# Performance work log

Measured on AMD Instinct MI355X. Metric: run time of the kernel, lower is better.

The kernel has to match this reference:

```python
import jax, jax.numpy as jnp
import numpy as np

B, T, M, VM = 64, 512, 8, 50  # batch, time, num_modules, rois per module
EPS = 1e-5  # BatchNorm eps


def setup_inputs() -> dict:
    key = jax.random.key(0)
    ks = jax.random.split(key, 12)
    x = jax.random.normal(ks[0], (B, M * VM, T, 1), jnp.float32)
    # learned adjacency, torch init = ones/V; perturb slightly
    PA = jnp.full((M, VM, VM), 1.0 / VM, jnp.float32) + 0.01 * jax.random.normal(ks[1], (M, VM, VM), jnp.float32)
    conv_w = jax.random.normal(ks[2], (M,), jnp.float32)          # 1x1 conv weight (1->1 chan) per module
    conv_b = 0.1 * jax.random.normal(ks[3], (M,), jnp.float32)
    bn_gamma = 1.0 + 0.1 * jax.random.normal(ks[4], (M,), jnp.float32)
    bn_beta = 0.1 * jax.random.normal(ks[5], (M,), jnp.float32)
    bn_mean = 0.1 * jax.random.normal(ks[6], (M,), jnp.float32)
    bn_var = jax.random.uniform(ks[7], (M,), jnp.float32) + 0.5   # positive
    w1 = jax.random.normal(ks[8], (M, 8), jnp.float32) * 0.5      # Linear(1,8) weight per module
    b1 = 0.1 * jax.random.normal(ks[9], (M, 8), jnp.float32)
    w2 = jax.random.normal(ks[10], (M, 8), jnp.float32) * 0.5     # Linear(8,1) weight per module
    b2 = 0.1 * jax.random.normal(ks[11], (M,), jnp.float32)
    return dict(x=x, PA=PA, conv_w=conv_w, conv_b=conv_b, bn_gamma=bn_gamma, bn_beta=bn_beta,
                bn_mean=bn_mean, bn_var=bn_var, w1=w1, b1=b1, w2=w2, b2=b2)


def reference(x, PA, conv_w, conv_b, bn_gamma, bn_beta, bn_mean, bn_var, w1, b1, w2, b2):
    # x: [B, V_total, T, 1]; torch permute(0,3,2,1) -> [B, C=1, T, V_total]
    xp = x[..., 0].transpose(0, 2, 1)                 # [B, T, V_total]
    xm = xp.reshape(B, T, M, VM)                      # contiguous module blocks == index_select
    # UnitGCN: x_agg = x @ A per module
    agg = jnp.einsum('btmv,mvw->btmw', xm, PA)        # [B, T, M, VM]
    # 1x1 conv (scalar per module) + BatchNorm2d(1) in eval mode + ReLU
    y = agg * conv_w[:, None] + conv_b[:, None]
    scale = bn_gamma / jnp.sqrt(bn_var + EPS)
    h = jax.nn.relu((y - bn_mean[:, None]) * scale[:, None] + bn_beta[:, None])
    # AttentionPooling: MLP(1->8->1) on channel dim, softmax over nodes, weighted sum
    hid = jnp.tanh(h[..., None] * w1[:, None, :] + b1[:, None, :])   # [B, T, M, VM, 8]
    score = jnp.einsum('btmvh,mh->btmv', hid, w2) + b2[:, None]      # [B, T, M, VM]
    attn = jax.nn.softmax(score, axis=3)
    pooled = jnp.sum(h * attn, axis=3)                # [B, T, M]
    # concat over modules on dim 1 -> [B, M, T, 1]
    return pooled.transpose(0, 2, 1)[..., None]
```

## Files before the change

### kernel.cpp

```cpp
#include <hip/hip_runtime.h>

#define BB 64
#define TT 512
#define MM 8
#define VMM 50
#define TBLK 128
#define RSTRIDE 36
#define EPSV 1e-5f

#define TN   1024
#define HMAX 16.0f
#define HSTEP (HMAX / TN)
#define INVH  (TN / HMAX)

using short8  = __attribute__((ext_vector_type(8))) short;
using float4v = __attribute__((ext_vector_type(4))) float;

__device__ __forceinline__ float fast_rcp(float x) {
    return __builtin_amdgcn_rcpf(x);
}
__device__ __forceinline__ float fast_tanh(float x) {
    float e2 = __expf(2.0f * x);
    return fmaf(-2.0f, fast_rcp(e2 + 1.0f), 1.0f);
}
__device__ __forceinline__ unsigned f2bf(float f) {
    unsigned u = __float_as_uint(f);
    return (u + 0x7FFFu + ((u >> 16) & 1u)) >> 16;
}
__device__ __forceinline__ unsigned pack2(float lo, float hi) {
    return f2bf(lo) | (f2bf(hi) << 16);
}
__device__ __forceinline__ unsigned packh2(float lo, float hi) {
    unsigned short a = __builtin_bit_cast(unsigned short, (_Float16)lo);
    unsigned short b = __builtin_bit_cast(unsigned short, (_Float16)hi);
    return (unsigned)a | ((unsigned)b << 16);
}
__device__ __forceinline__ float h2f_lo(unsigned p) {
    return (float)__builtin_bit_cast(_Float16, (unsigned short)(p & 0xFFFFu));
}
__device__ __forceinline__ float h2f_hi(unsigned p) {
    return (float)__builtin_bit_cast(_Float16, (unsigned short)(p >> 16));
}

__global__ __launch_bounds__(256)
__attribute__((amdgpu_waves_per_eu(4, 4)))
void intra_module_agg_kernel(const float* __restrict__ x,
                             const float* __restrict__ PA,
                             const float* __restrict__ conv_w,
                             const float* __restrict__ conv_b,
                             const float* __restrict__ bn_gamma,
                             const float* __restrict__ bn_beta,
                             const float* __restrict__ bn_mean,
                             const float* __restrict__ bn_var,
                             const float* __restrict__ w1,
                             const float* __restrict__ b1,
                             const float* __restrict__ w2,
                             const float* __restrict__ b2,
                             float* __restrict__ out)
{
    const int blk = blockIdx.x;
    const int tq  = blk & 3;
    const int m   = (blk >> 2) & 7;
    const int b   = blk >> 5;
    const int j   = threadIdx.x;

    const int lane = j & 63, wv = j >> 6;
    const int q = lane >> 4, nl = lane & 15;

    __shared__ __align__(16) unsigned psu[64 * RSTRIDE];
    __shared__ __align__(16) unsigned gt[TN];

    const float scale = bn_gamma[m] * __frsqrt_rn(bn_var[m] + EPSV);
    const float Amul  = conv_w[m] * scale;
    const float Cadd  = (conv_b[m] - bn_mean[m]) * scale + bn_beta[m];

    const int t0 = tq * TBLK;
    float xr[2][16];
#pragma unroll
    for (int t2 = 0; t2 < 2; ++t2) {
        const int t = t0 + (wv * 2 + t2) * 16 + nl;
        const float* xg = x + ((b * (MM * VMM) + m * VMM) * TT + t);
#pragma unroll
        for (int jj = 0; jj < 8; ++jj) {
            xr[t2][jj] = xg[(q * 8 + jj) * TT];
        }
#pragma unroll
        for (int jj = 0; jj < 8; ++jj) {
            int v  = 32 + q * 8 + jj;
            int vc = (v < VMM) ? v : 0;
            float tv = xg[vc * TT];
            xr[t2][8 + jj] = (v < VMM) ? tv : 0.0f;
        }
    }

    {
        const float* pa = PA + m * (VMM * VMM);
        const int w  = j & 63;
        const int vb = (j >> 6) * 8;
#pragma unroll
        for (int i = 0; i < 8; ++i) {
            int vp = vb + i, v0 = 2 * vp, v1 = v0 + 1;
            float a = (w < VMM && v0 < VMM) ? pa[v0 * VMM + w] : 0.0f;
            float c = (w < VMM && v1 < VMM) ? pa[v1 * VMM + w] : 0.0f;
            psu[w * RSTRIDE + vp] = pack2(a, c);
        }
    }

    {
        float W1[8], B1[8], W2[8];
        float B2 = b2[m], sabs = 0.0f;
#pragma unroll
        for (int k = 0; k < 8; ++k) {
            W1[k] = w1[m * 8 + k];
            B1[k] = b1[m * 8 + k];
            W2[k] = w2[m * 8 + k];
            sabs += fabsf(W2[k]);
        }
        const float s0 = (B2 + sabs) - 8.0f;
        float gv[5];
#pragma unroll
        for (int k = 0; k < 5; ++k) {
            float h = (4 * j + k) * HSTEP;
            float s = B2 - s0;
#pragma unroll
            for (int i = 0; i < 8; ++i)
                s = fmaf(W2[i], fast_tanh(fmaf(h, W1[i], B1[i])), s);
            gv[k] = __expf(s);
        }
#pragma unroll
        for (int k = 0; k < 4; ++k)
            gt[4 * j + k] = packh2(gv[k], gv[k + 1] - gv[k]);
    }

    short8 Bf[2][2];
#pragma unroll
    for (int t2 = 0; t2 < 2; ++t2) {
#pragma unroll
        for (int ks = 0; ks < 2; ++ks) {
            uint4 u;
            u.x = pack2(xr[t2][8 * ks + 0], xr[t2][8 * ks + 1]);
            u.y = pack2(xr[t2][8 * ks + 2], xr[t2][8 * ks + 3]);
            u.z = pack2(xr[t2][8 * ks + 4], xr[t2][8 * ks + 5]);
            u.w = pack2(xr[t2][8 * ks + 6], xr[t2][8 * ks + 7]);
            Bf[t2][ks] = __builtin_bit_cast(short8, u);
        }
    }

    __syncthreads();

    short8 A[4][2];
#pragma unroll
    for (int wt = 0; wt < 4; ++wt)
#pragma unroll
        for (int ks = 0; ks < 2; ++ks)
            A[wt][ks] = *(const short8*)&psu[(wt * 16 + nl) * RSTRIDE + ks * 16 + q * 4];

    float4v C[2][4];
#pragma unroll
    for (int t2 = 0; t2 < 2; ++t2)
#pragma unroll
        for (int wt = 0; wt < 4; ++wt)
            C[t2][wt] = (float4v){0.f, 0.f, 0.f, 0.f};

#pragma unroll
    for (int t2 = 0; t2 < 2; ++t2) {
#pragma unroll
        for (int wt = 0; wt < 4; ++wt) {
            C[t2][wt] = __builtin_amdgcn_mfma_f32_16x16x32_bf16(A[wt][0], Bf[t2][0], C[t2][wt], 0, 0, 0);
            C[t2][wt] = __builtin_amdgcn_mfma_f32_16x16x32_bf16(A[wt][1], Bf[t2][1], C[t2][wt], 0, 0, 0);
        }
    }

    const int obase = (b * MM + m) * TT + t0;
#pragma unroll
    for (int t2 = 0; t2 < 2; ++t2) {
        float se = 0.0f, sh = 0.0f;
#pragma unroll
        for (int wt = 0; wt < 4; ++wt) {
#pragma unroll
            for (int r = 0; r < 4; ++r) {
                const int w = wt * 16 + q * 4 + r;
                float h = fmaxf(fmaf(C[t2][wt][r], Amul, Cadd), 0.0f);
                float u = fminf(h, HMAX - 0.0005f) * INVH;
                int   i = (int)u;
                float fr = u - (float)i;
                unsigned p = gt[i];
                float e = (w < VMM) ? fmaf(fr, h2f_hi(p), h2f_lo(p)) : 0.0f;
                se += e;
                sh = fmaf(h, e, sh);
            }
        }
        se += __shfl_xor(se, 16, 64);
        se += __shfl_xor(se, 32, 64);
        sh += __shfl_xor(sh, 16, 64);
        sh += __shfl_xor(sh, 32, 64);
        if (q == 0)
            out[obase + (wv * 2 + t2) * 16 + nl] = sh * fast_rcp(se);
    }
}

extern "C" void kernel_launch(void* const* d_in, const int* in_sizes, int n_in,
                              void* d_out, int out_size, void* d_ws, size_t ws_size,
                              hipStream_t stream) {
    const float* x        = (const float*)d_in[0];
    const float* PA       = (const float*)d_in[1];
    const float* conv_w   = (const float*)d_in[2];
    const float* conv_b   = (const float*)d_in[3];
    const float* bn_gamma = (const float*)d_in[4];
    const float* bn_beta  = (const float*)d_in[5];
    const float* bn_mean  = (const float*)d_in[6];
    const float* bn_var   = (const float*)d_in[7];
    const float* w1       = (const float*)d_in[8];
    const float* b1       = (const float*)d_in[9];
    const float* w2       = (const float*)d_in[10];
    const float* b2       = (const float*)d_in[11];
    float* out = (float*)d_out;

    intra_module_agg_kernel<<<dim3(BB * MM * (TT / TBLK)), dim3(256), 0, stream>>>(
        x, PA, conv_w, conv_b, bn_gamma, bn_beta, bn_mean, bn_var,
        w1, b1, w2, b2, out);
}
```

Measured before the change: 115.2 us.

## Process full time axis per block with double-buffered register prefetch

Each block now handles all 512 timesteps of one (batch, module) pair instead of a 128-step quarter. The PA staging and exp lookup-table setup are done once per four tiles instead of once per tile. The next tile's loads are issued into a second register bank while the current tile runs its MFMA and softmax work. The grid shrinks from 2048 to 512 blocks and the waves-per-EU hint is relaxed to allow more registers, which may reduce occupancy and latency hiding.

```diff
diff --git a/kernel.cpp b/kernel.cpp
--- a/kernel.cpp
+++ b/kernel.cpp
@@ -4,7 +4,6 @@
 #define TT 512
 #define MM 8
 #define VMM 50
-#define TBLK 128
 #define RSTRIDE 36
 #define EPSV 1e-5f
 
@@ -42,8 +41,43 @@
     return (float)__builtin_bit_cast(_Float16, (unsigned short)(p >> 16));
 }
 
+__device__ __forceinline__ void load_tile(const float* __restrict__ xgb,
+                                          int t0, int wv, int nl, int q,
+                                          float xr[2][16])
+{
+#pragma unroll
+    for (int t2 = 0; t2 < 2; ++t2) {
+        const float* xg = xgb + t0 + (wv * 2 + t2) * 16 + nl;
+#pragma unroll
+        for (int jj = 0; jj < 8; ++jj)
+            xr[t2][jj] = xg[(q * 8 + jj) * TT];
+#pragma unroll
+        for (int jj = 0; jj < 8; ++jj) {
+            int v  = 32 + q * 8 + jj;
+            int vc = (v < VMM) ? v : 0;
+            float tv = xg[vc * TT];
+            xr[t2][8 + jj] = (v < VMM) ? tv : 0.0f;
+        }
+    }
+}
+
+__device__ __forceinline__ void pack_tile(const float xr[2][16], short8 Bf[2][2])
+{
+#pragma unroll
+    for (int t2 = 0; t2 < 2; ++t2)
+#pragma unroll
+        for (int ks = 0; ks < 2; ++ks) {
+            uint4 u;
+            u.x = pack2(xr[t2][8 * ks + 0], xr[t2][8 * ks + 1]);
+            u.y = pack2(xr[t2][8 * ks + 2], xr[t2][8 * ks + 3]);
+            u.z = pack2(xr[t2][8 * ks + 4], xr[t2][8 * ks + 5]);
+            u.w = pack2(xr[t2][8 * ks + 6], xr[t2][8 * ks + 7]);
+            Bf[t2][ks] = __builtin_bit_cast(short8, u);
+        }
+}
+
 __global__ __launch_bounds__(256)
-__attribute__((amdgpu_waves_per_eu(4, 4)))
+__attribute__((amdgpu_waves_per_eu(2)))
 void intra_module_agg_kernel(const float* __restrict__ x,
                              const float* __restrict__ PA,
                              const float* __restrict__ conv_w,
@@ -59,9 +93,8 @@
                              float* __restrict__ out)
 {
     const int blk = blockIdx.x;
-    const int tq  = blk & 3;
-    const int m   = (blk >> 2) & 7;
-    const int b   = blk >> 5;
+    const int m   = blk & 7;
+    const int b   = blk >> 3;
     const int j   = threadIdx.x;
 
     const int lane = j & 63, wv = j >> 6;
@@ -74,24 +107,11 @@
     const float Amul  = conv_w[m] * scale;
     const float Cadd  = (conv_b[m] - bn_mean[m]) * scale + bn_beta[m];
 
-    const int t0 = tq * TBLK;
-    float xr[2][16];
-#pragma unroll
-    for (int t2 = 0; t2 < 2; ++t2) {
-        const int t = t0 + (wv * 2 + t2) * 16 + nl;
-        const float* xg = x + ((b * (MM * VMM) + m * VMM) * TT + t);
-#pragma unroll
-        for (int jj = 0; jj < 8; ++jj) {
-            xr[t2][jj] = xg[(q * 8 + jj) * TT];
-        }
-#pragma unroll
-        for (int jj = 0; jj < 8; ++jj) {
-            int v  = 32 + q * 8 + jj;
-            int vc = (v < VMM) ? v : 0;
-            float tv = xg[vc * TT];
-            xr[t2][8 + jj] = (v < VMM) ? tv : 0.0f;
-        }
-    }
+    const float* xgb = x + ((b * (MM * VMM) + m * VMM) * TT);
+
+    float xr[2][2][16];
+    load_tile(xgb, 0 * 128, wv, nl, q, xr[0]);
+    load_tile(xgb, 1 * 128, wv, nl, q, xr[1]);
 
     {
         const float* pa = PA + m * (VMM * VMM);
@@ -132,21 +152,7 @@
             gt[4 * j + k] = packh2(gv[k], gv[k + 1] - gv[k]);
     }
 
-    short8 Bf[2][2];
-#pragma unroll
-    for (int t2 = 0; t2 < 2; ++t2) {
-#pragma unroll
-        for (int ks = 0; ks < 2; ++ks) {
-            uint4 u;
-            u.x = pack2(xr[t2][8 * ks + 0], xr[t2][8 * ks + 1]);
-            u.y = pack2(xr[t2][8 * ks + 2], xr[t2][8 * ks + 3]);
-            u.z = pack2(xr[t2][8 * ks + 4], xr[t2][8 * ks + 5]);
-            u.w = pack2(xr[t2][8 * ks + 6], xr[t2][8 * ks + 7]);
-            Bf[t2][ks] = __builtin_bit_cast(short8, u);
-        }
-    }
-
-    __syncthreads();
+    asm volatile("s_waitcnt lgkmcnt(0)\n\ts_barrier" ::: "memory");
 
     short8 A[4][2];
 #pragma unroll
@@ -155,47 +161,58 @@
         for (int ks = 0; ks < 2; ++ks)
             A[wt][ks] = *(const short8*)&psu[(wt * 16 + nl) * RSTRIDE + ks * 16 + q * 4];
 
-    float4v C[2][4];
-#pragma unroll
-    for (int t2 = 0; t2 < 2; ++t2)
-#pragma unroll
-        for (int wt = 0; wt < 4; ++wt)
-            C[t2][wt] = (float4v){0.f, 0.f, 0.f, 0.f};
-
-#pragma unroll
-    for (int t2 = 0; t2 < 2; ++t2) {
-#pragma unroll
-        for (int wt = 0; wt < 4; ++wt) {
-            C[t2][wt] = __builtin_amdgcn_mfma_f32_16x16x32_bf16(A[wt][0], Bf[t2][0], C[t2][wt], 0, 0, 0);
-            C[t2][wt] = __builtin_amdgcn_mfma_f32_16x16x32_bf16(A[wt][1], Bf[t2][1], C[t2][wt], 0, 0, 0);
-        }
-    }
-
-    const int obase = (b * MM + m) * TT + t0;
-#pragma unroll
-    for (int t2 = 0; t2 < 2; ++t2) {
-        float se = 0.0f, sh = 0.0f;
-#pragma unroll
-        for (int wt = 0; wt < 4; ++wt) {
-#pragma unroll
-            for (int r = 0; r < 4; ++r) {
-                const int w = wt * 16 + q * 4 + r;
-                float h = fmaxf(fmaf(C[t2][wt][r], Amul, Cadd), 0.0f);
-                float u = fminf(h, HMAX - 0.0005f) * INVH;
-                int   i = (int)u;
-                float fr = u - (float)i;
-                unsigned p = gt[i];
-                float e = (w < VMM) ? fmaf(fr, h2f_hi(p), h2f_lo(p)) : 0.0f;
-                se += e;
-                sh = fmaf(h, e, sh);
+    const int obase = (b * MM + m) * TT;
+#pragma unroll
+    for (int tl = 0; tl < 4; ++tl) {
+        const int bank = tl & 1;
+
+        short8 Bf[2][2];
+        pack_tile(xr[bank], Bf);
+
+        if (tl < 2)
+            load_tile(xgb, (tl + 2) * 128, wv, nl, q, xr[bank]);
+
+        float4v C[2][4];
+#pragma unroll
+        for (int t2 = 0; t2 < 2; ++t2)
+#pragma unroll
+            for (int wt = 0; wt < 4; ++wt)
+                C[t2][wt] = (float4v){0.f, 0.f, 0.f, 0.f};
+
+#pragma unroll
+        for (int t2 = 0; t2 < 2; ++t2)
+#pragma unroll
+            for (int wt = 0; wt < 4; ++wt) {
+                C[t2][wt] = __builtin_amdgcn_mfma_f32_16x16x32_bf16(A[wt][0], Bf[t2][0], C[t2][wt], 0, 0, 0);
+                C[t2][wt] = __builtin_amdgcn_mfma_f32_16x16x32_bf16(A[wt][1], Bf[t2][1], C[t2][wt], 0, 0, 0);
             }
-        }
-        se += __shfl_xor(se, 16, 64);
-        se += __shfl_xor(se, 32, 64);
-        sh += __shfl_xor(sh, 16, 64);
-        sh += __shfl_xor(sh, 32, 64);
-        if (q == 0)
-            out[obase + (wv * 2 + t2) * 16 + nl] = sh * fast_rcp(se);
+
+        const int ob = obase + tl * 128;
+#pragma unroll
+        for (int t2 = 0; t2 < 2; ++t2) {
+            float se = 0.0f, sh = 0.0f;
+#pragma unroll
+            for (int wt = 0; wt < 4; ++wt) {
+#pragma unroll
+                for (int r = 0; r < 4; ++r) {
+                    const int w = wt * 16 + q * 4 + r;
+                    float h = fmaxf(fmaf(C[t2][wt][r], Amul, Cadd), 0.0f);
+                    float u = fminf(h, HMAX - 0.0005f) * INVH;
+                    int   i = (int)u;
+                    float fr = u - (float)i;
+                    unsigned p = gt[i];
+                    float e = (w < VMM) ? fmaf(fr, h2f_hi(p), h2f_lo(p)) : 0.0f;
+                    se += e;
+                    sh = fmaf(h, e, sh);
+                }
+            }
+            se += __shfl_xor(se, 16, 64);
+            se += __shfl_xor(se, 32, 64);
+            sh += __shfl_xor(sh, 16, 64);
+            sh += __shfl_xor(sh, 32, 64);
+            if (q == 0)
+                out[ob + (wv * 2 + t2) * 16 + nl] = sh * fast_rcp(se);
+        }
     }
 }
 
@@ -216,7 +233,7 @@
     const float* b2       = (const float*)d_in[11];
     float* out = (float*)d_out;
 
-    intra_module_agg_kernel<<<dim3(BB * MM * (TT / TBLK)), dim3(256), 0, stream>>>(
+    intra_module_agg_kernel<<<dim3(BB * MM), dim3(256), 0, stream>>>(
         x, PA, conv_w, conv_b, bn_gamma, bn_beta, bn_mean, bn_var,
         w1, b1, w2, b2, out);
 }
```

Measured after the change: 110.1 us. 4.4% less time.
